# Kernel optimization log

Measured on AMD Instinct MI355X. Metric: run time of the kernel, lower is better.

The kernel has to match this reference:

```python
import jax, jax.numpy as jnp
import numpy as np

N, E, D, H, C, G, L = 100000, 1600000, 128, 4, 32, 4096, 3  # nodes, edges, h_dim, heads, head_dim, graphs, conv blocks


def setup_inputs() -> dict:
    key = jax.random.key(0)
    ks = jax.random.split(key, 24)
    s = 0.05
    w = lambda k, shape: jax.random.normal(k, shape, jnp.float32) * s
    inp = {
        "x": jax.random.normal(ks[0], (N, D), jnp.float32),
        "edge_index": jax.random.randint(ks[1], (2, E), 0, N),
        "batch": jnp.sort(jax.random.randint(ks[2], (N,), 0, G)),
        # input TransformerConv (in=D, out=C per head, H heads, beta=True)
        "in_Wq": w(ks[3], (D, D)), "in_bq": jnp.zeros((D,), jnp.float32),
        "in_Wk": w(ks[4], (D, D)), "in_bk": jnp.zeros((D,), jnp.float32),
        "in_Wv": w(ks[5], (D, D)), "in_bv": jnp.zeros((D,), jnp.float32),
        "in_Ws": w(ks[6], (D, D)), "in_bs": jnp.zeros((D,), jnp.float32),
        "in_Wbeta": w(ks[7], (3 * D,)),
        # stacked conv blocks (L of them, in=out=D)
        "blk_Wq": w(ks[8], (L, D, D)), "blk_bq": jnp.zeros((L, D), jnp.float32),
        "blk_Wk": w(ks[9], (L, D, D)), "blk_bk": jnp.zeros((L, D), jnp.float32),
        "blk_Wv": w(ks[10], (L, D, D)), "blk_bv": jnp.zeros((L, D), jnp.float32),
        "blk_Ws": w(ks[11], (L, D, D)), "blk_bs": jnp.zeros((L, D), jnp.float32),
        "blk_Wbeta": w(ks[12], (L, 3 * D)),
        # MLP head
        "W1": w(ks[13], (D, 64)), "b1": jnp.zeros((64,), jnp.float32),
        "W2": w(ks[14], (64, 32)), "b2": jnp.zeros((32,), jnp.float32),
        "W3": w(ks[15], (32, 1)), "b3": jnp.zeros((1,), jnp.float32),
    }
    return inp


def transformer_conv(x, src, dst, Wq, bq, Wk, bk, Wv, bv, Ws, bs, Wbeta):
    # PyG TransformerConv, concat=True, root_weight=True, beta=True, eval mode
    q = (x @ Wq + bq).reshape(N, H, C)
    k = (x @ Wk + bk).reshape(N, H, C)
    v = (x @ Wv + bv).reshape(N, H, C)
    # per-edge attention logits: message j=src -> i=dst
    alpha = jnp.einsum("ehc,ehc->eh", q[dst], k[src]) / jnp.sqrt(jnp.float32(C))  # [E,H]
    m = jax.ops.segment_max(alpha, dst, num_segments=N)
    m = jnp.where(jnp.isfinite(m), m, 0.0)
    e = jnp.exp(alpha - m[dst])
    denom = jax.ops.segment_sum(e, dst, num_segments=N)
    a = e / (denom[dst] + 1e-16)  # segment softmax over in-edges of dst
    msg = a[..., None] * v[src]  # [E,H,C]
    out = jax.ops.segment_sum(msg, dst, num_segments=N).reshape(N, H * C)
    x_r = x @ Ws + bs
    beta = jax.nn.sigmoid(jnp.concatenate([out, x_r, out - x_r], axis=-1) @ Wbeta)[:, None]
    return beta * x_r + (1.0 - beta) * out


def reference(x, edge_index, batch, in_Wq, in_bq, in_Wk, in_bk, in_Wv, in_bv,
              in_Ws, in_bs, in_Wbeta, blk_Wq, blk_bq, blk_Wk, blk_bk, blk_Wv,
              blk_bv, blk_Ws, blk_bs, blk_Wbeta, W1, b1, W2, b2, W3, b3):
    src, dst = edge_index[0], edge_index[1]
    h = jax.nn.relu(transformer_conv(x, src, dst, in_Wq, in_bq, in_Wk, in_bk,
                                     in_Wv, in_bv, in_Ws, in_bs, in_Wbeta))
    for l in range(L):  # dropout is identity in eval mode
        h = jax.nn.relu(transformer_conv(h, src, dst, blk_Wq[l], blk_bq[l],
                                         blk_Wk[l], blk_bk[l], blk_Wv[l], blk_bv[l],
                                         blk_Ws[l], blk_bs[l], blk_Wbeta[l]))
    # global mean pool over graphs
    sums = jax.ops.segment_sum(h, batch, num_segments=G)
    cnt = jax.ops.segment_sum(jnp.ones((N, 1), h.dtype), batch, num_segments=G)
    g = sums / jnp.maximum(cnt, 1.0)
    g = jax.nn.relu(g @ W1 + b1)
    g = jax.nn.relu(g @ W2 + b2)
    return jax.nn.sigmoid(g @ W3 + b3)
```

## Files before the change

### kernel.cpp

```cpp
#include <hip/hip_runtime.h>
#include <hip/hip_bf16.h>
#include <cstdint>

#define DH 128
#define NB 256
#define NBK 1024

typedef __attribute__((ext_vector_type(8))) short short8;
typedef __attribute__((ext_vector_type(4))) float floatx4;
typedef __attribute__((ext_vector_type(2))) float floatx2;

__device__ __forceinline__ float bflo(unsigned u) { return __uint_as_float(u << 16); }
__device__ __forceinline__ float bfhi(unsigned u) { return __uint_as_float(u & 0xffff0000u); }

__device__ __forceinline__ unsigned pk_bf16(float a, float b) {
  return ((unsigned)__bfloat16_as_ushort(__float2bfloat16(b)) << 16)
       | (unsigned)__bfloat16_as_ushort(__float2bfloat16(a));
}

template<int CTRL>
__device__ __forceinline__ float dpp_add(float x) {
  int y = __builtin_amdgcn_update_dpp(0, __float_as_int(x), CTRL, 0xf, 0xf, true);
  return x + __int_as_float(y);
}


__global__ void cvt_bf16(const float* __restrict__ x, __hip_bfloat16* __restrict__ o, int n) {
  int i = blockIdx.x * 256 + threadIdx.x;
  if (i < n) o[i] = __float2bfloat16(x[i]);
}


__global__ void scan1_kernel(const int* __restrict__ deg, int* __restrict__ off,
                             int* __restrict__ bsum, int n) {
  __shared__ int sh[256];
  int idx = blockIdx.x * 256 + threadIdx.x;
  int v = (idx < n) ? deg[idx] : 0;
  sh[threadIdx.x] = v;
  __syncthreads();
  for (int d = 1; d < 256; d <<= 1) {
    int x = (threadIdx.x >= (unsigned)d) ? sh[threadIdx.x - d] : 0;
    __syncthreads();
    sh[threadIdx.x] += x;
    __syncthreads();
  }
  if (idx < n) off[idx] = sh[threadIdx.x] - v;
  if (threadIdx.x == 255) bsum[blockIdx.x] = sh[255];
}

__global__ void scan2_kernel(int* __restrict__ bsum, int nb) {
  __shared__ int sh[512];
  int t = threadIdx.x;
  int v = (t < nb) ? bsum[t] : 0;
  sh[t] = v;
  __syncthreads();
  for (int d = 1; d < 512; d <<= 1) {
    int x = (t >= (unsigned)d) ? sh[t - d] : 0;
    __syncthreads();
    sh[t] += x;
    __syncthreads();
  }
  if (t < nb) bsum[t] = sh[t] - v;
}

__global__ void scan3_kernel(int* __restrict__ off, const int* __restrict__ bsum, int n) {
  int idx = blockIdx.x * 256 + threadIdx.x;
  if (idx < n) off[idx] += bsum[blockIdx.x];
}


__global__ __launch_bounds__(256)
void csr_p1(const int* __restrict__ dst, int* __restrict__ hist, int E, int chunk) {
  __shared__ int cnt[NBK];
  const int blk = blockIdx.x, tid = threadIdx.x;
  for (int c = tid; c < NBK; c += 256) cnt[c] = 0;
  __syncthreads();
  int base = blk * chunk;
  int end = base + chunk; if (end > E) end = E;
  for (int e = base + tid; e < end; e += 256) atomicAdd(&cnt[dst[e] >> 7], 1);
  __syncthreads();
  for (int c = tid; c < NBK; c += 256) hist[c * NB + blk] = cnt[c];
}

__global__ __launch_bounds__(256)
void csr_p2(int* __restrict__ hist, int* __restrict__ total) {
  int b = blockIdx.x * 4 + (threadIdx.x >> 6);
  int lane = threadIdx.x & 63;
  int4 v = *(int4*)&hist[b * NB + lane * 4];
  int s0 = v.x;
  int s1 = s0 + v.y;
  int s2 = s1 + v.z;
  int s3 = s2 + v.w;
  int t = s3;
  for (int d = 1; d < 64; d <<= 1) {
    int y = __shfl_up(t, d);
    if (lane >= d) t += y;
  }
  int excl = t - s3;
  int4 o;
  o.x = excl; o.y = excl + s0; o.z = excl + s1; o.w = excl + s2;
  *(int4*)&hist[b * NB + lane * 4] = o;
  if (lane == 63) total[b] = t;
}

__global__ __launch_bounds__(256)
void csr_p3(const int* __restrict__ src, const int* __restrict__ dst,
            const int* __restrict__ hist, const int* __restrict__ tstart,
            int* __restrict__ part, int E, int chunk) {
  __shared__ int cur[NBK];
  const int blk = blockIdx.x, tid = threadIdx.x;
  for (int c = tid; c < NBK; c += 256) cur[c] = hist[c * NB + blk] + tstart[c];
  __syncthreads();
  int base = blk * chunk;
  int end = base + chunk; if (end > E) end = E;
  for (int e = base + tid; e < end; e += 256) {
    int d = dst[e];
    int b = d >> 7;
    int pos = atomicAdd(&cur[b], 1);
    part[pos] = (src[e] << 7) | (d & 127);
  }
}

__global__ __launch_bounds__(256)
void csr_p4(const int* __restrict__ part, const int* __restrict__ tstart,
            const int* __restrict__ total, int* __restrict__ deg,
            int* __restrict__ off, int* __restrict__ csr, int Nn) {
  __shared__ int lcnt[128], lscan[128], lcur[128];
  const int b = blockIdx.x, tid = threadIdx.x;
  const int p0 = tstart[b];
  const int m = total[b];
  if (tid < 128) lcnt[tid] = 0;
  __syncthreads();
  for (int k = tid; k < m; k += 256) atomicAdd(&lcnt[part[p0 + k] & 127], 1);
  __syncthreads();
  if (tid < 128) lscan[tid] = lcnt[tid];
  __syncthreads();
  for (int d = 1; d < 128; d <<= 1) {
    int v = 0;
    if (tid < 128 && tid >= d) v = lscan[tid - d];
    __syncthreads();
    if (tid < 128) lscan[tid] += v;
    __syncthreads();
  }
  if (tid < 128) {
    int ex = lscan[tid] - lcnt[tid];
    lcur[tid] = ex;
    int n = (b << 7) + tid;
    if (n < Nn) { deg[n] = lcnt[tid]; off[n] = p0 + ex; }
  }
  __syncthreads();
  for (int k = tid; k < m; k += 256) {
    int pk = part[p0 + k];
    int pos = p0 + atomicAdd(&lcur[pk & 127], 1);
    csr[pos] = pk >> 7;
  }
}


__global__ void goff_kernel(const int* __restrict__ batch, int* __restrict__ goff,
                            int N, int G) {
  int g = blockIdx.x * 256 + threadIdx.x;
  if (g > G) return;
  if (g == G) { goff[G] = N; return; }
  int lo = 0, hi = N;
  while (lo < hi) { int mid = (lo + hi) >> 1; if (batch[mid] < g) lo = mid + 1; else hi = mid; }
  goff[g] = lo;
}


__global__ __launch_bounds__(256)
void pack_w_kernel(const float* __restrict__ Wq, const float* __restrict__ Wk,
                   const float* __restrict__ Wv, const float* __restrict__ Ws,
                   const float* __restrict__ bq, const float* __restrict__ bk,
                   const float* __restrict__ bv, const float* __restrict__ bs,
                   __hip_bfloat16* __restrict__ WT2, float* __restrict__ bcat) {
  if (blockIdx.x == 64) {
    for (int c = threadIdx.x; c < 512; c += 256) {
      int which = c >> 7, cc = c & 127;
      const float* b = (which == 0) ? bq : (which == 1) ? bk : (which == 2) ? bv : bs;
      bcat[c] = b[cc];
    }
    return;
  }
  __shared__ float tile[32][33];
  const int bid = blockIdx.x;
  const int which = bid >> 4, kb = (bid >> 2) & 3, cb = bid & 3;
  const float* W = (which == 0) ? Wq : (which == 1) ? Wk : (which == 2) ? Wv : Ws;
  const int tx = threadIdx.x & 31, ty = threadIdx.x >> 5;
#pragma unroll
  for (int r = ty; r < 32; r += 8)
    tile[r][tx] = W[(kb * 32 + r) * 128 + cb * 32 + tx];
  __syncthreads();
  const int t = threadIdx.x;
  const int mt_sel = t >> 7;
  const int s4 = (t & 127) * 4;
  const int l16 = s4 >> 5;
  const int quad = (s4 >> 3) & 3;
  const int j0 = s4 & 7;
  const int cl = mt_sel * 16 + l16;
  const int kr = quad * 8 + j0;
  float f0 = tile[kr + 0][cl];
  float f1 = tile[kr + 1][cl];
  float f2 = tile[kr + 2][cl];
  float f3 = tile[kr + 3][cl];
  const int mt = which * 8 + cb * 2 + mt_sel;
  const int o = mt * 2048 + kb * 512 + l16 * 32 + quad * 8 + j0;
  uint2 w;
  w.x = pk_bf16(f0, f1);
  w.y = pk_bf16(f2, f3);
  *(uint2*)&((unsigned short*)WT2)[o] = w;
}


__global__ __launch_bounds__(256)
void gemm_qkvs(const short* __restrict__ Xb, const short* __restrict__ WT2,
               const float* __restrict__ bc,
               unsigned int* __restrict__ qout,
               unsigned int* __restrict__ kvp,
               unsigned int* __restrict__ xrout, int Nn) {
  __shared__ short As[32][132];
  const int row0 = blockIdx.x * 32;
  const int tid = threadIdx.x;

#pragma unroll
  for (int p = 0; p < 2; ++p) {
    int chunk = p * 256 + tid;
    int r = chunk >> 4, c8 = chunk & 15;
    int row = row0 + r; if (row >= Nn) row = Nn - 1;
    *(int4*)&As[r][c8 * 8] = *(const int4*)&Xb[(size_t)row * 128 + c8 * 8];
  }
  __syncthreads();

  const int w = tid >> 6, lane = tid & 63, quad = lane >> 4, l16 = lane & 15;

  short8 xf[2][4];
#pragma unroll
  for (int nt = 0; nt < 2; ++nt)
#pragma unroll
    for (int kt = 0; kt < 4; ++kt)
      xf[nt][kt] = *(const short8*)&As[nt * 16 + l16][kt * 32 + quad * 8];

  const int fbase = l16 * 32 + quad * 8;

  if (w == 0 || w == 3) {
    unsigned int* outp = (w == 0) ? qout : xrout;
    const int mbase = (w == 0) ? 0 : 24;
#pragma unroll
    for (int i = 0; i < 8; ++i) {
      const int mt = mbase + i;
      short8 af[4];
#pragma unroll
      for (int kt = 0; kt < 4; ++kt)
        af[kt] = *(const short8*)&WT2[mt * 2048 + kt * 512 + fbase];
      float4 bias = *(const float4*)&bc[mt * 16 + quad * 4];
      const int wc = (i * 16 + quad * 4);
#pragma unroll
      for (int nt = 0; nt < 2; ++nt) {
        floatx4 acc = (floatx4){0.f, 0.f, 0.f, 0.f};
#pragma unroll
        for (int kt = 0; kt < 4; ++kt)
          acc = __builtin_amdgcn_mfma_f32_16x16x32_bf16(af[kt], xf[nt][kt], acc, 0, 0, 0);
        int node = row0 + nt * 16 + l16;
        if (node < Nn) {
          uint2 o;
          o.x = pk_bf16(acc[0] + bias.x, acc[1] + bias.y);
          o.y = pk_bf16(acc[2] + bias.z, acc[3] + bias.w);
          *(uint2*)&outp[(size_t)node * 64 + (wc >> 1)] = o;
        }
      }
    }
  } else {
    const int kb = 8 + (w - 1) * 4;
    const int vb = 16 + (w - 1) * 4;
#pragma unroll
    for (int i = 0; i < 4; ++i) {
      const int mk = kb + i, mv = vb + i;
      short8 afk[4], afv[4];
#pragma unroll
      for (int kt = 0; kt < 4; ++kt) {
        afk[kt] = *(const short8*)&WT2[mk * 2048 + kt * 512 + fbase];
        afv[kt] = *(const short8*)&WT2[mv * 2048 + kt * 512 + fbase];
      }
      float4 bk4 = *(const float4*)&bc[mk * 16 + quad * 4];
      float4 bv4 = *(const float4*)&bc[mv * 16 + quad * 4];
      const int krel = (w - 1) * 64 + i * 16 + quad * 4;
#pragma unroll
      for (int nt = 0; nt < 2; ++nt) {
        floatx4 ak = (floatx4){0.f, 0.f, 0.f, 0.f};
        floatx4 av = (floatx4){0.f, 0.f, 0.f, 0.f};
#pragma unroll
        for (int kt = 0; kt < 4; ++kt) {
          ak = __builtin_amdgcn_mfma_f32_16x16x32_bf16(afk[kt], xf[nt][kt], ak, 0, 0, 0);
          av = __builtin_amdgcn_mfma_f32_16x16x32_bf16(afv[kt], xf[nt][kt], av, 0, 0, 0);
        }
        int node = row0 + nt * 16 + l16;
        if (node < Nn) {
          int d0 = __builtin_amdgcn_cvt_pk_fp8_f32(ak[0] + bk4.x, ak[1] + bk4.y, 0, false);
          d0 = __builtin_amdgcn_cvt_pk_fp8_f32(av[0] + bv4.x, av[1] + bv4.y, d0, true);
          int d1 = __builtin_amdgcn_cvt_pk_fp8_f32(ak[2] + bk4.z, ak[3] + bk4.w, 0, false);
          d1 = __builtin_amdgcn_cvt_pk_fp8_f32(av[2] + bv4.z, av[3] + bv4.w, d1, true);
          uint2 o; o.x = (unsigned)d0; o.y = (unsigned)d1;
          *(uint2*)&kvp[(size_t)node * 64 + (krel >> 1)] = o;
        }
      }
    }
  }
}


__global__ __launch_bounds__(256)
void attn_kernel(unsigned int* __restrict__ q_h, const uint4* __restrict__ kvq,
                 const uint4* __restrict__ xr4, const int* __restrict__ off,
                 const int* __restrict__ deg, const int* __restrict__ csr,
                 const float* __restrict__ Wb, int Nn) {
  int wv = __builtin_amdgcn_readfirstlane(threadIdx.x >> 6);
  int i = blockIdx.x * 4 + wv;
  if (i >= Nn) return;
  const int l = threadIdx.x & 63;
  const int j = l & 15;
  const int g = l >> 4;

  const float QS = 0.17677669529663687f * 1.4426950408889634f;
  uint4 qw = ((const uint4*)q_h)[(size_t)i * 16 + j];
  float q0 = bflo(qw.x) * QS, q1 = bfhi(qw.x) * QS;
  float q2 = bflo(qw.y) * QS, q3 = bfhi(qw.y) * QS;
  float q4 = bflo(qw.z) * QS, q5 = bfhi(qw.z) * QS;
  float q6 = bflo(qw.w) * QS, q7 = bfhi(qw.w) * QS;

  const int e0 = off[i];
  const int dg = deg[i];
  const int eend = e0 + dg;

  float denA = 0.f, denB = 0.f;
  float aA[8] = {0.f, 0.f, 0.f, 0.f, 0.f, 0.f, 0.f, 0.f};
  float aB[8] = {0.f, 0.f, 0.f, 0.f, 0.f, 0.f, 0.f, 0.f};

  auto comp = [&](const uint4& kv, bool valid, float& den, float (&a)[8]) {
    floatx2 k0 = __builtin_amdgcn_cvt_pk_f32_fp8((int)kv.x, false);
    floatx2 v0 = __builtin_amdgcn_cvt_pk_f32_fp8((int)kv.x, true);
    floatx2 k1 = __builtin_amdgcn_cvt_pk_f32_fp8((int)kv.y, false);
    floatx2 v1 = __builtin_amdgcn_cvt_pk_f32_fp8((int)kv.y, true);
    floatx2 k2 = __builtin_amdgcn_cvt_pk_f32_fp8((int)kv.z, false);
    floatx2 v2 = __builtin_amdgcn_cvt_pk_f32_fp8((int)kv.z, true);
    floatx2 k3 = __builtin_amdgcn_cvt_pk_f32_fp8((int)kv.w, false);
    floatx2 v3 = __builtin_amdgcn_cvt_pk_f32_fp8((int)kv.w, true);
    float d = q0 * k0.x + q1 * k0.y + q2 * k1.x + q3 * k1.y
            + q4 * k2.x + q5 * k2.y + q6 * k3.x + q7 * k3.y;
    d = dpp_add<0xB1>(d);
    d = dpp_add<0x4E>(d);
    float p = valid ? exp2f(d) : 0.f;
    den += p;
    a[0] += p * v0.x; a[1] += p * v0.y; a[2] += p * v1.x; a[3] += p * v1.y;
    a[4] += p * v2.x; a[5] += p * v2.y; a[6] += p * v3.x; a[7] += p * v3.y;
  };

  for (int e = e0; e < eend; e += 64) {
    const int rem = eend - e;
    const int take = (rem < 64) ? rem : 64;
    int il = e + l; if (il >= eend) il = eend - 1;
    const int sv = csr[il];

    for (int b = 0; b < take; b += 16) {
      uint4 kv0, kv1, kv2, kv3;
      bool p0 = false, p1 = false, p2 = false, p3 = false;
      const int c0 = b + g, c1 = b + 4 + g, c2 = b + 8 + g, c3 = b + 12 + g;
      {
        p0 = c0 < take;
        int s = __shfl(sv, p0 ? c0 : 0);
        kv0 = kvq[(unsigned)((s << 4) | j)];
      }
      if (b + 4 < take) {
        p1 = c1 < take;
        int s = __shfl(sv, p1 ? c1 : 0);
        kv1 = kvq[(unsigned)((s << 4) | j)];
      }
      if (b + 8 < take) {
        p2 = c2 < take;
        int s = __shfl(sv, p2 ? c2 : 0);
        kv2 = kvq[(unsigned)((s << 4) | j)];
      }
      if (b + 12 < take) {
        p3 = c3 < take;
        int s = __shfl(sv, p3 ? c3 : 0);
        kv3 = kvq[(unsigned)((s << 4) | j)];
      }
      comp(kv0, p0, denA, aA);
      if (b + 4 < take)  comp(kv1, p1, denB, aB);
      if (b + 8 < take)  comp(kv2, p2, denA, aA);
      if (b + 12 < take) comp(kv3, p3, denB, aB);
    }
  }

  uint4 xw = xr4[(size_t)i * 16 + j];
  float4 wo0 = *(const float4*)&Wb[8 * j];
  float4 wo1 = *(const float4*)&Wb[8 * j + 4];
  float4 wx0 = *(const float4*)&Wb[128 + 8 * j];
  float4 wx1 = *(const float4*)&Wb[128 + 8 * j + 4];
  float4 wd0 = *(const float4*)&Wb[256 + 8 * j];
  float4 wd1 = *(const float4*)&Wb[256 + 8 * j + 4];

  float den = denA + denB;
  float a0 = aA[0] + aB[0], a1 = aA[1] + aB[1], a2 = aA[2] + aB[2], a3 = aA[3] + aB[3];
  float a4 = aA[4] + aB[4], a5 = aA[5] + aB[5], a6 = aA[6] + aB[6], a7 = aA[7] + aB[7];

  den += __shfl_xor(den, 16); den += __shfl_xor(den, 32);
  a0 += __shfl_xor(a0, 16); a0 += __shfl_xor(a0, 32);
  a1 += __shfl_xor(a1, 16); a1 += __shfl_xor(a1, 32);
  a2 += __shfl_xor(a2, 16); a2 += __shfl_xor(a2, 32);
  a3 += __shfl_xor(a3, 16); a3 += __shfl_xor(a3, 32);
  a4 += __shfl_xor(a4, 16); a4 += __shfl_xor(a4, 32);
  a5 += __shfl_xor(a5, 16); a5 += __shfl_xor(a5, 32);
  a6 += __shfl_xor(a6, 16); a6 += __shfl_xor(a6, 32);
  a7 += __shfl_xor(a7, 16); a7 += __shfl_xor(a7, 32);

  float inv = 1.f / (den + 1e-16f);
  float o0 = a0 * inv, o1 = a1 * inv, o2 = a2 * inv, o3 = a3 * inv;
  float o4 = a4 * inv, o5 = a5 * inv, o6 = a6 * inv, o7 = a7 * inv;

  float x0 = bflo(xw.x), x1 = bfhi(xw.x);
  float x2 = bflo(xw.y), x3 = bfhi(xw.y);
  float x4 = bflo(xw.z), x5 = bfhi(xw.z);
  float x6 = bflo(xw.w), x7 = bfhi(xw.w);

  float c = o0 * wo0.x + o1 * wo0.y + o2 * wo0.z + o3 * wo0.w
          + o4 * wo1.x + o5 * wo1.y + o6 * wo1.z + o7 * wo1.w
          + x0 * wx0.x + x1 * wx0.y + x2 * wx0.z + x3 * wx0.w
          + x4 * wx1.x + x5 * wx1.y + x6 * wx1.z + x7 * wx1.w
          + (o0 - x0) * wd0.x + (o1 - x1) * wd0.y + (o2 - x2) * wd0.z + (o3 - x3) * wd0.w
          + (o4 - x4) * wd1.x + (o5 - x5) * wd1.y + (o6 - x6) * wd1.z + (o7 - x7) * wd1.w;
  c = dpp_add<0xB1>(c);
  c = dpp_add<0x4E>(c);
  c = dpp_add<0x141>(c);
  c = dpp_add<0x140>(c);
  float beta = 1.f / (1.f + __expf(-c));

  if (g == 0) {
    float h0 = fmaxf(beta * x0 + (1.f - beta) * o0, 0.f);
    float h1 = fmaxf(beta * x1 + (1.f - beta) * o1, 0.f);
    float h2 = fmaxf(beta * x2 + (1.f - beta) * o2, 0.f);
    float h3 = fmaxf(beta * x3 + (1.f - beta) * o3, 0.f);
    float h4 = fmaxf(beta * x4 + (1.f - beta) * o4, 0.f);
    float h5 = fmaxf(beta * x5 + (1.f - beta) * o5, 0.f);
    float h6 = fmaxf(beta * x6 + (1.f - beta) * o6, 0.f);
    float h7 = fmaxf(beta * x7 + (1.f - beta) * o7, 0.f);
    uint4 hw;
    hw.x = pk_bf16(h0, h1);
    hw.y = pk_bf16(h2, h3);
    hw.z = pk_bf16(h4, h5);
    hw.w = pk_bf16(h6, h7);
    ((uint4*)q_h)[(size_t)i * 16 + j] = hw;
  }
}


__global__ __launch_bounds__(128)
void poolmlp_kernel(const unsigned short* __restrict__ h, const int* __restrict__ goff,
                    const float* __restrict__ W1, const float* __restrict__ b1,
                    const float* __restrict__ W2, const float* __restrict__ b2,
                    const float* __restrict__ W3, const float* __restrict__ b3,
                    float* __restrict__ out) {
  int g = blockIdx.x;
  int t = threadIdx.x;
  int n0 = goff[g], cnt = goff[g + 1] - n0;
  float s = 0.f;
  for (int n = n0; n < n0 + cnt; ++n) s += bflo(h[(size_t)n * 128 + t]);
  __shared__ float gv[128];
  __shared__ float t1[64];
  __shared__ float t2[32];
  gv[t] = s / fmaxf((float)cnt, 1.0f);
  __syncthreads();
  if (t < 64) {
    float a = b1[t];
    for (int k = 0; k < 128; ++k) a += gv[k] * W1[k * 64 + t];
    t1[t] = fmaxf(a, 0.f);
  }
  __syncthreads();
  if (t < 32) {
    float a = b2[t];
    for (int k = 0; k < 64; ++k) a += t1[k] * W2[k * 32 + t];
    t2[t] = fmaxf(a, 0.f);
  }
  __syncthreads();
  if (t == 0) {
    float a = b3[0];
    for (int k = 0; k < 32; ++k) a += t2[k] * W3[k];
    out[g] = 1.f / (1.f + __expf(-a));
  }
}


extern "C" void kernel_launch(void* const* d_in, const int* in_sizes, int n_in,
                              void* d_out, int out_size, void* d_ws, size_t ws_size,
                              hipStream_t stream) {
  const float* x = (const float*)d_in[0];
  const int* edge_index = (const int*)d_in[1];
  const int* batch = (const int*)d_in[2];
  const int N = in_sizes[0] / DH;
  const int E = in_sizes[1] / 2;
  const int G = out_size;
  const int* src = edge_index;
  const int* dst = edge_index + E;

  const float* in_Wq = (const float*)d_in[3];
  const float* in_bq = (const float*)d_in[4];
  const float* in_Wk = (const float*)d_in[5];
  const float* in_bk = (const float*)d_in[6];
  const float* in_Wv = (const float*)d_in[7];
  const float* in_bv = (const float*)d_in[8];
  const float* in_Ws = (const float*)d_in[9];
  const float* in_bs = (const float*)d_in[10];
  const float* in_Wbeta = (const float*)d_in[11];
  const float* blk_Wq = (const float*)d_in[12];
  const float* blk_bq = (const float*)d_in[13];
  const float* blk_Wk = (const float*)d_in[14];
  const float* blk_bk = (const float*)d_in[15];
  const float* blk_Wv = (const float*)d_in[16];
  const float* blk_bv = (const float*)d_in[17];
  const float* blk_Ws = (const float*)d_in[18];
  const float* blk_bs = (const float*)d_in[19];
  const float* blk_Wbeta = (const float*)d_in[20];

  char* p = (char*)d_ws;
  auto take = [&](size_t bytes) { char* r = p; p += (bytes + 255) & ~(size_t)255; return r; };
  __hip_bfloat16* h0 = (__hip_bfloat16*)take((size_t)N * DH * 2);
  __hip_bfloat16* h1 = (__hip_bfloat16*)take((size_t)N * DH * 2);
  unsigned char* kvp = (unsigned char*)take((size_t)N * 256);
  unsigned short* xr = (unsigned short*)take((size_t)N * DH * 2);
  __hip_bfloat16* WT2 = (__hip_bfloat16*)take((size_t)512 * DH * 2);
  float* bcat = (float*)take(512 * 4);
  int* deg    = (int*)take((size_t)N * 4);
  int* off    = (int*)take((size_t)N * 4);
  int* csr    = (int*)take((size_t)E * 4);
  int* part   = (int*)take((size_t)E * 4);
  int* hist   = (int*)take((size_t)NB * NBK * 4);
  int* total  = (int*)take(NBK * 4);
  int* tstart = (int*)take(NBK * 4);
  int* bsumP  = (int*)take(512 * 4);
  int* goff   = (int*)take((size_t)(G + 1) * 4);
  (void)n_in;
  if ((size_t)(p - (char*)d_ws) > ws_size) return;

  const int NBUCK = (N + 127) >> 7;
  const int chunk = (E + NB - 1) / NB;

  csr_p1<<<NB, 256, 0, stream>>>(dst, hist, E, chunk);
  csr_p2<<<NBK / 4, 256, 0, stream>>>(hist, total);
  scan1_kernel<<<NBK / 256, 256, 0, stream>>>(total, tstart, bsumP, NBK);
  scan2_kernel<<<1, 512, 0, stream>>>(bsumP, NBK / 256);
  scan3_kernel<<<NBK / 256, 256, 0, stream>>>(tstart, bsumP, NBK);
  csr_p3<<<NB, 256, 0, stream>>>(src, dst, hist, tstart, part, E, chunk);
  csr_p4<<<NBUCK, 256, 0, stream>>>(part, tstart, total, deg, off, csr, N);

  goff_kernel<<<(G + 256) / 256, 256, 0, stream>>>(batch, goff, N, G);

  cvt_bf16<<<(int)(((size_t)N * DH + 255) / 256), 256, 0, stream>>>(x, h0, N * DH);

  for (int l = 0; l < 4; ++l) {
    const float *Wq, *Wk, *Wv, *Ws, *bq, *bk, *bv, *bs, *Wb;
    if (l == 0) {
      Wq = in_Wq; Wk = in_Wk; Wv = in_Wv; Ws = in_Ws;
      bq = in_bq; bk = in_bk; bv = in_bv; bs = in_bs; Wb = in_Wbeta;
    } else {
      int m = l - 1;
      Wq = blk_Wq + (size_t)m * DH * DH; Wk = blk_Wk + (size_t)m * DH * DH;
      Wv = blk_Wv + (size_t)m * DH * DH; Ws = blk_Ws + (size_t)m * DH * DH;
      bq = blk_bq + (size_t)m * DH; bk = blk_bk + (size_t)m * DH;
      bv = blk_bv + (size_t)m * DH; bs = blk_bs + (size_t)m * DH;
      Wb = blk_Wbeta + (size_t)m * 3 * DH;
    }
    __hip_bfloat16* hin  = (l & 1) ? h1 : h0;
    __hip_bfloat16* qbuf = (l & 1) ? h0 : h1;
    pack_w_kernel<<<65, 256, 0, stream>>>(Wq, Wk, Wv, Ws, bq, bk, bv, bs, WT2, bcat);
    gemm_qkvs<<<(N + 31) / 32, 256, 0, stream>>>((const short*)hin, (const short*)WT2, bcat,
        (unsigned int*)qbuf, (unsigned int*)kvp, (unsigned int*)xr, N);
    attn_kernel<<<(N + 3) / 4, 256, 0, stream>>>((unsigned int*)qbuf, (const uint4*)kvp,
        (const uint4*)xr, off, deg, csr, Wb, N);
  }

  poolmlp_kernel<<<G, 128, 0, stream>>>((const unsigned short*)h0, goff,
      (const float*)d_in[21], (const float*)d_in[22],
      (const float*)d_in[23], (const float*)d_in[24],
      (const float*)d_in[25], (const float*)d_in[26],
      (float*)d_out);
}
```

Baseline: 711.6 us.

## Fuse input conversion into GEMM, batch weight packing, merge scans, deepen attention gather

The three-kernel scan over bucket totals becomes a single 1024-thread block scan. Weight packing for all four layers now runs in one launch before the layer loop. The fp32-to-bf16 conversion of x is folded into the first layer's GEMM load. The attention kernel moves from 4 to 2 waves per block and issues up to 8 independent key/value gathers per iteration instead of 4, exposing more memory-level parallelism at the cost of extra registers.

```diff
diff --git a/kernel.cpp b/kernel.cpp
--- a/kernel.cpp
+++ b/kernel.cpp
@@ -22,50 +22,6 @@
 __device__ __forceinline__ float dpp_add(float x) {
   int y = __builtin_amdgcn_update_dpp(0, __float_as_int(x), CTRL, 0xf, 0xf, true);
   return x + __int_as_float(y);
-}
-
-
-__global__ void cvt_bf16(const float* __restrict__ x, __hip_bfloat16* __restrict__ o, int n) {
-  int i = blockIdx.x * 256 + threadIdx.x;
-  if (i < n) o[i] = __float2bfloat16(x[i]);
-}
-
-
-__global__ void scan1_kernel(const int* __restrict__ deg, int* __restrict__ off,
-                             int* __restrict__ bsum, int n) {
-  __shared__ int sh[256];
-  int idx = blockIdx.x * 256 + threadIdx.x;
-  int v = (idx < n) ? deg[idx] : 0;
-  sh[threadIdx.x] = v;
-  __syncthreads();
-  for (int d = 1; d < 256; d <<= 1) {
-    int x = (threadIdx.x >= (unsigned)d) ? sh[threadIdx.x - d] : 0;
-    __syncthreads();
-    sh[threadIdx.x] += x;
-    __syncthreads();
-  }
-  if (idx < n) off[idx] = sh[threadIdx.x] - v;
-  if (threadIdx.x == 255) bsum[blockIdx.x] = sh[255];
-}
-
-__global__ void scan2_kernel(int* __restrict__ bsum, int nb) {
-  __shared__ int sh[512];
-  int t = threadIdx.x;
-  int v = (t < nb) ? bsum[t] : 0;
-  sh[t] = v;
-  __syncthreads();
-  for (int d = 1; d < 512; d <<= 1) {
-    int x = (t >= (unsigned)d) ? sh[t - d] : 0;
-    __syncthreads();
-    sh[t] += x;
-    __syncthreads();
-  }
-  if (t < nb) bsum[t] = sh[t] - v;
-}
-
-__global__ void scan3_kernel(int* __restrict__ off, const int* __restrict__ bsum, int n) {
-  int idx = blockIdx.x * 256 + threadIdx.x;
-  if (idx < n) off[idx] += bsum[blockIdx.x];
 }
 
 
@@ -103,6 +59,22 @@
   if (lane == 63) total[b] = t;
 }
 
+__global__ __launch_bounds__(1024)
+void scan_tstart(const int* __restrict__ total, int* __restrict__ tstart) {
+  __shared__ int sh[1024];
+  int t = threadIdx.x;
+  int v = total[t];
+  sh[t] = v;
+  __syncthreads();
+  for (int d = 1; d < 1024; d <<= 1) {
+    int x = (t >= d) ? sh[t - d] : 0;
+    __syncthreads();
+    sh[t] += x;
+    __syncthreads();
+  }
+  tstart[t] = sh[t] - v;
+}
+
 __global__ __launch_bounds__(256)
 void csr_p3(const int* __restrict__ src, const int* __restrict__ dst,
             const int* __restrict__ hist, const int* __restrict__ tstart,
@@ -169,21 +141,39 @@
 
 
 __global__ __launch_bounds__(256)
-void pack_w_kernel(const float* __restrict__ Wq, const float* __restrict__ Wk,
-                   const float* __restrict__ Wv, const float* __restrict__ Ws,
-                   const float* __restrict__ bq, const float* __restrict__ bk,
-                   const float* __restrict__ bv, const float* __restrict__ bs,
+void pack_w_kernel(const float* __restrict__ iWq, const float* __restrict__ iWk,
+                   const float* __restrict__ iWv, const float* __restrict__ iWs,
+                   const float* __restrict__ ibq, const float* __restrict__ ibk,
+                   const float* __restrict__ ibv, const float* __restrict__ ibs,
+                   const float* __restrict__ bWq, const float* __restrict__ bWk,
+                   const float* __restrict__ bWv, const float* __restrict__ bWs,
+                   const float* __restrict__ bbq, const float* __restrict__ bbk,
+                   const float* __restrict__ bbv, const float* __restrict__ bbs,
                    __hip_bfloat16* __restrict__ WT2, float* __restrict__ bcat) {
-  if (blockIdx.x == 64) {
+  const int layer = blockIdx.x / 65;
+  const int bid = blockIdx.x % 65;
+  const float *Wq, *Wk, *Wv, *Ws, *bq, *bk, *bv, *bs;
+  if (layer == 0) {
+    Wq = iWq; Wk = iWk; Wv = iWv; Ws = iWs; bq = ibq; bk = ibk; bv = ibv; bs = ibs;
+  } else {
+    int m = layer - 1;
+    Wq = bWq + (size_t)m * DH * DH; Wk = bWk + (size_t)m * DH * DH;
+    Wv = bWv + (size_t)m * DH * DH; Ws = bWs + (size_t)m * DH * DH;
+    bq = bbq + (size_t)m * DH; bk = bbk + (size_t)m * DH;
+    bv = bbv + (size_t)m * DH; bs = bbs + (size_t)m * DH;
+  }
+  unsigned short* WT2l = (unsigned short*)WT2 + (size_t)layer * 65536;
+  float* bcl = bcat + layer * 512;
+
+  if (bid == 64) {
     for (int c = threadIdx.x; c < 512; c += 256) {
       int which = c >> 7, cc = c & 127;
       const float* b = (which == 0) ? bq : (which == 1) ? bk : (which == 2) ? bv : bs;
-      bcat[c] = b[cc];
+      bcl[c] = b[cc];
     }
     return;
   }
   __shared__ float tile[32][33];
-  const int bid = blockIdx.x;
   const int which = bid >> 4, kb = (bid >> 2) & 3, cb = bid & 3;
   const float* W = (which == 0) ? Wq : (which == 1) ? Wk : (which == 2) ? Wv : Ws;
   const int tx = threadIdx.x & 31, ty = threadIdx.x >> 5;
@@ -208,12 +198,13 @@
   uint2 w;
   w.x = pk_bf16(f0, f1);
   w.y = pk_bf16(f2, f3);
-  *(uint2*)&((unsigned short*)WT2)[o] = w;
-}
-
-
+  *(uint2*)&WT2l[o] = w;
+}
+
+
+template<int F32IN>
 __global__ __launch_bounds__(256)
-void gemm_qkvs(const short* __restrict__ Xb, const short* __restrict__ WT2,
+void gemm_qkvs(const void* __restrict__ Xin, const short* __restrict__ WT2,
                const float* __restrict__ bc,
                unsigned int* __restrict__ qout,
                unsigned int* __restrict__ kvp,
@@ -227,7 +218,19 @@
     int chunk = p * 256 + tid;
     int r = chunk >> 4, c8 = chunk & 15;
     int row = row0 + r; if (row >= Nn) row = Nn - 1;
-    *(int4*)&As[r][c8 * 8] = *(const int4*)&Xb[(size_t)row * 128 + c8 * 8];
+    if (F32IN) {
+      const float* xf = (const float*)Xin + (size_t)row * 128 + c8 * 8;
+      float4 f0 = *(const float4*)xf;
+      float4 f1 = *(const float4*)(xf + 4);
+      int4 pk;
+      ((unsigned*)&pk)[0] = pk_bf16(f0.x, f0.y);
+      ((unsigned*)&pk)[1] = pk_bf16(f0.z, f0.w);
+      ((unsigned*)&pk)[2] = pk_bf16(f1.x, f1.y);
+      ((unsigned*)&pk)[3] = pk_bf16(f1.z, f1.w);
+      *(int4*)&As[r][c8 * 8] = pk;
+    } else {
+      *(int4*)&As[r][c8 * 8] = *(const int4*)((const short*)Xin + (size_t)row * 128 + c8 * 8);
+    }
   }
   __syncthreads();
 
@@ -308,13 +311,13 @@
 }
 
 
-__global__ __launch_bounds__(256)
+__global__ __launch_bounds__(128)
 void attn_kernel(unsigned int* __restrict__ q_h, const uint4* __restrict__ kvq,
                  const uint4* __restrict__ xr4, const int* __restrict__ off,
                  const int* __restrict__ deg, const int* __restrict__ csr,
                  const float* __restrict__ Wb, int Nn) {
   int wv = __builtin_amdgcn_readfirstlane(threadIdx.x >> 6);
-  int i = blockIdx.x * 4 + wv;
+  int i = blockIdx.x * 2 + wv;
   if (i >= Nn) return;
   const int l = threadIdx.x & 63;
   const int j = l & 15;
@@ -360,34 +363,26 @@
     int il = e + l; if (il >= eend) il = eend - 1;
     const int sv = csr[il];
 
-    for (int b = 0; b < take; b += 16) {
-      uint4 kv0, kv1, kv2, kv3;
-      bool p0 = false, p1 = false, p2 = false, p3 = false;
-      const int c0 = b + g, c1 = b + 4 + g, c2 = b + 8 + g, c3 = b + 12 + g;
-      {
-        p0 = c0 < take;
-        int s = __shfl(sv, p0 ? c0 : 0);
-        kv0 = kvq[(unsigned)((s << 4) | j)];
+    for (int base = 0; base < take; base += 32) {
+      const int left = take - base;
+      const int ns = (left + 3) >> 2 < 8 ? (left + 3) >> 2 : 8;
+      int sarr[8];
+      bool pv[8];
+#pragma unroll
+      for (int u = 0; u < 8; ++u) {
+        if (u < ns) {
+          int c = base + u * 4 + g;
+          pv[u] = c < take;
+          sarr[u] = __shfl(sv, pv[u] ? c : 0);
+        }
       }
-      if (b + 4 < take) {
-        p1 = c1 < take;
-        int s = __shfl(sv, p1 ? c1 : 0);
-        kv1 = kvq[(unsigned)((s << 4) | j)];
-      }
-      if (b + 8 < take) {
-        p2 = c2 < take;
-        int s = __shfl(sv, p2 ? c2 : 0);
-        kv2 = kvq[(unsigned)((s << 4) | j)];
-      }
-      if (b + 12 < take) {
-        p3 = c3 < take;
-        int s = __shfl(sv, p3 ? c3 : 0);
-        kv3 = kvq[(unsigned)((s << 4) | j)];
-      }
-      comp(kv0, p0, denA, aA);
-      if (b + 4 < take)  comp(kv1, p1, denB, aB);
-      if (b + 8 < take)  comp(kv2, p2, denA, aA);
-      if (b + 12 < take) comp(kv3, p3, denB, aB);
+      uint4 kv[8];
+#pragma unroll
+      for (int u = 0; u < 8; ++u)
+        if (u < ns) kv[u] = kvq[(unsigned)((sarr[u] << 4) | j)];
+#pragma unroll
+      for (int u = 0; u < 8; ++u)
+        if (u < ns) comp(kv[u], pv[u], (u & 1) ? denB : denA, (u & 1) ? aB : aA);
     }
   }
 
@@ -526,8 +521,8 @@
   __hip_bfloat16* h1 = (__hip_bfloat16*)take((size_t)N * DH * 2);
   unsigned char* kvp = (unsigned char*)take((size_t)N * 256);
   unsigned short* xr = (unsigned short*)take((size_t)N * DH * 2);
-  __hip_bfloat16* WT2 = (__hip_bfloat16*)take((size_t)512 * DH * 2);
-  float* bcat = (float*)take(512 * 4);
+  __hip_bfloat16* WT2 = (__hip_bfloat16*)take((size_t)4 * 512 * DH * 2);
+  float* bcat = (float*)take((size_t)4 * 512 * 4);
   int* deg    = (int*)take((size_t)N * 4);
   int* off    = (int*)take((size_t)N * 4);
   int* csr    = (int*)take((size_t)E * 4);
@@ -535,7 +530,6 @@
   int* hist   = (int*)take((size_t)NB * NBK * 4);
   int* total  = (int*)take(NBK * 4);
   int* tstart = (int*)take(NBK * 4);
-  int* bsumP  = (int*)take(512 * 4);
   int* goff   = (int*)take((size_t)(G + 1) * 4);
   (void)n_in;
   if ((size_t)(p - (char*)d_ws) > ws_size) return;
@@ -545,35 +539,31 @@
 
   csr_p1<<<NB, 256, 0, stream>>>(dst, hist, E, chunk);
   csr_p2<<<NBK / 4, 256, 0, stream>>>(hist, total);
-  scan1_kernel<<<NBK / 256, 256, 0, stream>>>(total, tstart, bsumP, NBK);
-  scan2_kernel<<<1, 512, 0, stream>>>(bsumP, NBK / 256);
-  scan3_kernel<<<NBK / 256, 256, 0, stream>>>(tstart, bsumP, NBK);
+  scan_tstart<<<1, 1024, 0, stream>>>(total, tstart);
   csr_p3<<<NB, 256, 0, stream>>>(src, dst, hist, tstart, part, E, chunk);
   csr_p4<<<NBUCK, 256, 0, stream>>>(part, tstart, total, deg, off, csr, N);
 
   goff_kernel<<<(G + 256) / 256, 256, 0, stream>>>(batch, goff, N, G);
 
-  cvt_bf16<<<(int)(((size_t)N * DH + 255) / 256), 256, 0, stream>>>(x, h0, N * DH);
+  pack_w_kernel<<<4 * 65, 256, 0, stream>>>(
+      in_Wq, in_Wk, in_Wv, in_Ws, in_bq, in_bk, in_bv, in_bs,
+      blk_Wq, blk_Wk, blk_Wv, blk_Ws, blk_bq, blk_bk, blk_bv, blk_bs,
+      WT2, bcat);
 
   for (int l = 0; l < 4; ++l) {
-    const float *Wq, *Wk, *Wv, *Ws, *bq, *bk, *bv, *bs, *Wb;
-    if (l == 0) {
-      Wq = in_Wq; Wk = in_Wk; Wv = in_Wv; Ws = in_Ws;
-      bq = in_bq; bk = in_bk; bv = in_bv; bs = in_bs; Wb = in_Wbeta;
-    } else {
-      int m = l - 1;
-      Wq = blk_Wq + (size_t)m * DH * DH; Wk = blk_Wk + (size_t)m * DH * DH;
-      Wv = blk_Wv + (size_t)m * DH * DH; Ws = blk_Ws + (size_t)m * DH * DH;
-      bq = blk_bq + (size_t)m * DH; bk = blk_bk + (size_t)m * DH;
-      bv = blk_bv + (size_t)m * DH; bs = blk_bs + (size_t)m * DH;
-      Wb = blk_Wbeta + (size_t)m * 3 * DH;
-    }
+    const float* Wb = (l == 0) ? in_Wbeta : blk_Wbeta + (size_t)(l - 1) * 3 * DH;
+    const short* WT2l = (const short*)WT2 + (size_t)l * 65536;
+    const float* bcl = bcat + (size_t)l * 512;
     __hip_bfloat16* hin  = (l & 1) ? h1 : h0;
     __hip_bfloat16* qbuf = (l & 1) ? h0 : h1;
-    pack_w_kernel<<<65, 256, 0, stream>>>(Wq, Wk, Wv, Ws, bq, bk, bv, bs, WT2, bcat);
-    gemm_qkvs<<<(N + 31) / 32, 256, 0, stream>>>((const short*)hin, (const short*)WT2, bcat,
-        (unsigned int*)qbuf, (unsigned int*)kvp, (unsigned int*)xr, N);
-    attn_kernel<<<(N + 3) / 4, 256, 0, stream>>>((unsigned int*)qbuf, (const uint4*)kvp,
+    if (l == 0) {
+      gemm_qkvs<1><<<(N + 31) / 32, 256, 0, stream>>>((const void*)x, WT2l, bcl,
+          (unsigned int*)qbuf, (unsigned int*)kvp, (unsigned int*)xr, N);
+    } else {
+      gemm_qkvs<0><<<(N + 31) / 32, 256, 0, stream>>>((const void*)hin, WT2l, bcl,
+          (unsigned int*)qbuf, (unsigned int*)kvp, (unsigned int*)xr, N);
+    }
+    attn_kernel<<<(N + 1) / 2, 128, 0, stream>>>((unsigned int*)qbuf, (const uint4*)kvp,
         (const uint4*)xr, off, deg, csr, Wb, N);
   }
 
```

Measured after the change: 788.6 us. 10.8% more time.
